# Kernel optimization log

Measured on AMD Instinct MI355X. Metric: run time of the kernel, lower is better.

Reference implementation:

```python
import jax, jax.numpy as jnp
import numpy as np

N_NODES = 10000
IN_SIZE, H_SIZE, OUT_SIZE = 512, 512, 64
N_EDGES = 163840


def gcn_conv(x, edge_index, W, b, n_nodes):
    """PyG-style GCNConv: add self-loops, sym-normalize, x @ W, scatter-add, + bias."""
    src, dst = edge_index[0], edge_index[1]
    loop = jnp.arange(n_nodes, dtype=src.dtype)
    src = jnp.concatenate([src, loop])
    dst = jnp.concatenate([dst, loop])
    # degree over destinations (self-loops included)
    deg = jax.ops.segment_sum(jnp.ones_like(dst, dtype=x.dtype), dst, num_segments=n_nodes)
    dinv = jnp.where(deg > 0, jax.lax.rsqrt(deg), 0.0)
    norm = dinv[src] * dinv[dst]                      # [E+N]
    h = x @ W                                          # [N, out]
    msg = h[src] * norm[:, None]                       # gather + scale
    out = jax.ops.segment_sum(msg, dst, num_segments=n_nodes)  # scatter-add
    return out + b


def setup_inputs() -> dict:
    key = jax.random.key(0)
    k = jax.random.split(key, 6)
    x = jax.random.normal(k[0], (N_NODES, IN_SIZE), dtype=jnp.float32)
    edge_index = jax.random.randint(k[1], (2, N_EDGES), 0, N_NODES, dtype=jnp.int64 if jax.config.read('jax_enable_x64') else jnp.int32)
    # Glorot-ish init for weights, zero bias (PyG default)
    W1 = jax.random.normal(k[2], (IN_SIZE, H_SIZE), dtype=jnp.float32) * (1.0 / np.sqrt(IN_SIZE))
    b1 = jnp.zeros((H_SIZE,), dtype=jnp.float32)
    W2 = jax.random.normal(k[3], (H_SIZE, OUT_SIZE), dtype=jnp.float32) * (1.0 / np.sqrt(H_SIZE))
    b2 = jnp.zeros((OUT_SIZE,), dtype=jnp.float32)
    return {"x": x, "edge_index": edge_index, "W1": W1, "b1": b1, "W2": W2, "b2": b2}


def reference(x, edge_index, W1, b1, W2, b2):
    n = x.shape[0]
    h = gcn_conv(x, edge_index, W1, b1, n)
    h = jax.nn.relu(h)
    h = gcn_conv(h, edge_index, W2, b2, n)
    return (h, jax.nn.log_softmax(h, axis=1))
```

## Files before the change

kernel.cpp:

```cpp
#include <hip/hip_runtime.h>
#include <math.h>

#define NN 10000
#define INF 512
#define HF  512
#define OF  64
#define NE  163840
#define MAXDEG 64

typedef __attribute__((ext_vector_type(8))) short bf16x8_t;
typedef __attribute__((ext_vector_type(4))) float f32x4_t;

__device__ inline ushort f2bf(float f) {
    unsigned u = __float_as_uint(f);
    u = (u + 0x7FFF + ((u >> 16) & 1)) >> 16;
    return (ushort)u;
}
__device__ inline float bf2f(ushort u) {
    return __uint_as_float(((unsigned)u) << 16);
}

#define GLL(gp, lp) __builtin_amdgcn_global_load_lds(                         \
    (const __attribute__((address_space(1))) unsigned int*)(gp),              \
    (__attribute__((address_space(3))) unsigned int*)(lp), 16, 0, 0)

#define CCB_X  2500
#define CCB_W1 2756
#define CCB_W2 2788
#define CCB_Z  2828
__global__ __launch_bounds__(256) void k_cvt(const float* __restrict__ X,
                                             ushort* __restrict__ Xb,
                                             const float* __restrict__ W1,
                                             ushort* __restrict__ W1T,
                                             const float* __restrict__ W2,
                                             ushort* __restrict__ W2T,
                                             int* __restrict__ gdeg) {
    __shared__ float tl[32][33];
    int b = blockIdx.x, t = threadIdx.x;
    if (b < CCB_X) {
        int i = (b * 256 + t) * 2;
        const float4* Xv = (const float4*)X;
        float4 v0 = Xv[i], v1 = Xv[i + 1];
        ushort4 o0, o1;
        o0.x = f2bf(v0.x); o0.y = f2bf(v0.y); o0.z = f2bf(v0.z); o0.w = f2bf(v0.w);
        o1.x = f2bf(v1.x); o1.y = f2bf(v1.y); o1.z = f2bf(v1.z); o1.w = f2bf(v1.w);
        ((ushort4*)Xb)[i] = o0;
        ((ushort4*)Xb)[i + 1] = o1;
    } else if (b < CCB_W2) {
        const float* W; ushort* WT; int N, tile;
        if (b < CCB_W1) { W = W1; WT = W1T; N = 512; tile = b - CCB_X; }
        else            { W = W2; WT = W2T; N = 64;  tile = b - CCB_W1; }
        int k0 = (tile & 15) * 32;
        int n0 = (tile >> 4) * 32;
        int tx = t & 31, ty = t >> 5;
#pragma unroll
        for (int i = 0; i < 4; i++)
            tl[ty + i * 8][tx] = W[(size_t)(k0 + ty + i * 8) * N + n0 + tx];
        __syncthreads();
#pragma unroll
        for (int i = 0; i < 4; i++)
            WT[(size_t)(n0 + ty + i * 8) * 512 + k0 + tx] = f2bf(tl[tx][ty + i * 8]);
    } else {
        int i = (b - CCB_W2) * 256 + t;
        if (i < NN) gdeg[i] = 0;
    }
}

#define GEMM_B 316
__global__ __launch_bounds__(256) void k_gemm_ell(const ushort* __restrict__ Xb,
                                                  const ushort* __restrict__ WT,
                                                  ushort* __restrict__ Y,
                                                  const int* __restrict__ src,
                                                  const int* __restrict__ dst,
                                                  int* __restrict__ gdeg,
                                                  int* __restrict__ ell, int E) {
    __shared__ ushort As[128 * 128];
    __shared__ ushort Bs[128 * 128];
    int b = blockIdx.x;
    int tid = threadIdx.x;
    if (b >= GEMM_B) {
        int e = (b - GEMM_B) * 256 + tid;
        if (e < E) {
            int s = src[e], d = dst[e];
            int r = atomicAdd(&gdeg[d], 1);
            if (r < MAXDEG) ell[d * MAXDEG + r] = s;
        }
        return;
    }
    int lane = tid & 63;
    int wave = tid >> 6;
    int m = lane & 15;
    int q = lane >> 4;
    int wr = wave >> 1;
    int wc = wave & 1;
    int row0 = (b % 79) * 128;
    int col0 = (b / 79) * 128;

    int lrow = lane >> 4;
    int p = lane & 15;
    int koff[4];
#pragma unroll
    for (int jm = 0; jm < 4; jm++) koff[jm] = (p ^ ((jm * 4 + lrow) & 15)) * 8;

    f32x4_t acc[4][4];
#pragma unroll
    for (int r = 0; r < 4; r++)
#pragma unroll
        for (int c = 0; c < 4; c++) acc[r][c] = (f32x4_t){0.f, 0.f, 0.f, 0.f};

    for (int kb = 0; kb < 512; kb += 128) {
#pragma unroll
        for (int j = 0; j < 8; j++) {
            int rloc = wave * 32 + j * 4;
            GLL(Xb + (size_t)(row0 + rloc + lrow) * 512 + kb + koff[j & 3],
                As + rloc * 128);
            GLL(WT + (size_t)(col0 + rloc + lrow) * 512 + kb + koff[j & 3],
                Bs + rloc * 128);
        }
        __syncthreads();
#pragma unroll
        for (int kc = 0; kc < 4; kc++) {
            bf16x8_t a[4], bb[4];
            int slot = ((kc * 4 + q) ^ m) * 8;
#pragma unroll
            for (int r = 0; r < 4; r++)
                a[r] = *(const bf16x8_t*)(As + (wr * 64 + r * 16 + m) * 128 + slot);
#pragma unroll
            for (int c = 0; c < 4; c++)
                bb[c] = *(const bf16x8_t*)(Bs + (wc * 64 + c * 16 + m) * 128 + slot);
#pragma unroll
            for (int r = 0; r < 4; r++)
#pragma unroll
                for (int c = 0; c < 4; c++)
                    acc[r][c] = __builtin_amdgcn_mfma_f32_16x16x32_bf16(a[r], bb[c], acc[r][c], 0, 0, 0);
        }
        __syncthreads();
    }
#pragma unroll
    for (int r = 0; r < 4; r++) {
#pragma unroll
        for (int c = 0; c < 4; c++) {
#pragma unroll
            for (int reg = 0; reg < 4; reg++) {
                int row = row0 + wr * 64 + r * 16 + q * 4 + reg;
                int col = col0 + wc * 64 + c * 16 + m;
                if (row < NN) Y[(size_t)row * 512 + col] = f2bf(acc[r][c][reg]);
            }
        }
    }
}

__global__ __launch_bounds__(256) void k_gemm64_mfma(const ushort* __restrict__ Ab,
                                                     const ushort* __restrict__ W2T,
                                                     ushort* __restrict__ Y) {
    __shared__ ushort As[64 * 128];
    __shared__ ushort Bs[64 * 128];
    int tid = threadIdx.x;
    int lane = tid & 63;
    int wave = tid >> 6;
    int m = lane & 15;
    int q = lane >> 4;
    int row0 = blockIdx.x * 64;

    int lrow = lane >> 4;
    int p = lane & 15;
    int koff[4];
#pragma unroll
    for (int jm = 0; jm < 4; jm++) koff[jm] = (p ^ ((jm * 4 + lrow) & 15)) * 8;

    f32x4_t acc[4];
#pragma unroll
    for (int c = 0; c < 4; c++) acc[c] = (f32x4_t){0.f, 0.f, 0.f, 0.f};

    for (int kb = 0; kb < 512; kb += 128) {
#pragma unroll
        for (int j = 0; j < 4; j++) {
            int rloc = wave * 16 + j * 4;
            GLL(Ab + (size_t)(row0 + rloc + lrow) * 512 + kb + koff[j],
                As + rloc * 128);
            GLL(W2T + (size_t)(rloc + lrow) * 512 + kb + koff[j],
                Bs + rloc * 128);
        }
        __syncthreads();
#pragma unroll
        for (int kc = 0; kc < 4; kc++) {
            int slot = ((kc * 4 + q) ^ m) * 8;
            bf16x8_t a = *(const bf16x8_t*)(As + (wave * 16 + m) * 128 + slot);
#pragma unroll
            for (int c = 0; c < 4; c++) {
                bf16x8_t bfr = *(const bf16x8_t*)(Bs + (c * 16 + m) * 128 + slot);
                acc[c] = __builtin_amdgcn_mfma_f32_16x16x32_bf16(a, bfr, acc[c], 0, 0, 0);
            }
        }
        __syncthreads();
    }
#pragma unroll
    for (int c = 0; c < 4; c++) {
#pragma unroll
        for (int reg = 0; reg < 4; reg++) {
            int row = row0 + wave * 16 + q * 4 + reg;
            int col = c * 16 + m;
            if (row < NN) Y[(size_t)row * 64 + col] = f2bf(acc[c][reg]);
        }
    }
}

__global__ __launch_bounds__(256) void k_agg1(const ushort* __restrict__ h1b,
                                              const int* __restrict__ gdeg,
                                              const int* __restrict__ ell,
                                              const float* __restrict__ b,
                                              ushort* __restrict__ a1b,
                                              float* __restrict__ wts) {
    __shared__ int   sidx[64];
    __shared__ float swt[64];
    int v = blockIdx.x;
    int t = threadIdx.x;
    int deg = gdeg[v]; if (deg > MAXDEG) deg = MAXDEG;
    float dv = rsqrtf((float)(deg + 1));
    if (t < 64) {
        int s = 0; float wt = 0.f;
        if (t < deg) {
            s = ell[v * MAXDEG + t];
            wt = rsqrtf((float)(gdeg[s] + 1)) * dv;
        }
        sidx[t] = s; swt[t] = wt;
        wts[v * MAXDEG + t] = wt;
    }
    __syncthreads();

    int fb = t * 2;
    float ax[8], ay[8];
#pragma unroll
    for (int k = 0; k < 8; k++) { ax[k] = 0.f; ay[k] = 0.f; }
    {
        ushort2 u = *(const ushort2*)(h1b + (size_t)v * 512 + fb);
        float dv2 = dv * dv;
        ax[0] = bf2f(u.x) * dv2;
        ay[0] = bf2f(u.y) * dv2;
    }
    int nr = (deg + 7) & ~7;
    for (int i = 0; i < nr; i += 8) {
        int   sK[8]; float wK[8];
#pragma unroll
        for (int k = 0; k < 8; k++) { sK[k] = sidx[i + k]; wK[k] = swt[i + k]; }
#pragma unroll
        for (int k = 0; k < 8; k++) {
            ushort2 u = *(const ushort2*)(h1b + (size_t)sK[k] * 512 + fb);
            ax[k] += bf2f(u.x) * wK[k];
            ay[k] += bf2f(u.y) * wK[k];
        }
    }
    float tx = ((ax[0] + ax[1]) + (ax[2] + ax[3])) + ((ax[4] + ax[5]) + (ax[6] + ax[7]));
    float ty = ((ay[0] + ay[1]) + (ay[2] + ay[3])) + ((ay[4] + ay[5]) + (ay[6] + ay[7]));
    tx += b[fb];
    ty += b[fb + 1];
    ushort2 o;
    o.x = f2bf(tx > 0.f ? tx : 0.f);
    o.y = f2bf(ty > 0.f ? ty : 0.f);
    *(ushort2*)(a1b + (size_t)v * 512 + fb) = o;
}

__global__ __launch_bounds__(256) void k_agg2_lsm(const ushort* __restrict__ h2b,
                                                  const int* __restrict__ gdeg,
                                                  const int* __restrict__ ell,
                                                  const float* __restrict__ wts,
                                                  const float* __restrict__ b,
                                                  float* __restrict__ out) {
    __shared__ int   sidx[4][64];
    __shared__ float swt[4][64];
    int t = threadIdx.x & 63;
    int w = threadIdx.x >> 6;
    int v = blockIdx.x * 4 + w;
    int deg = gdeg[v]; if (deg > MAXDEG) deg = MAXDEG;
    float dv = rsqrtf((float)(deg + 1));
    int   e_ = ell[v * MAXDEG + t];
    float w_ = wts[v * MAXDEG + t];
    sidx[w][t] = (t < deg) ? e_ : 0;
    swt[w][t]  = (t < deg) ? w_ : 0.f;

    float acc[8];
#pragma unroll
    for (int k = 0; k < 8; k++) acc[k] = 0.f;
    acc[0] = bf2f(h2b[(size_t)v * 64 + t]) * (dv * dv);

    int nr = (deg + 7) & ~7;
    for (int i = 0; i < nr; i += 8) {
        int   sK[8]; float wK[8];
#pragma unroll
        for (int k = 0; k < 8; k++) { sK[k] = sidx[w][i + k]; wK[k] = swt[w][i + k]; }
#pragma unroll
        for (int k = 0; k < 8; k++)
            acc[k] += bf2f(h2b[(size_t)sK[k] * 64 + t]) * wK[k];
    }
    float h = ((acc[0] + acc[1]) + (acc[2] + acc[3])) +
              ((acc[4] + acc[5]) + (acc[6] + acc[7]));
    h += b[t];
    out[(size_t)v * 64 + t] = h;
    float m = h;
#pragma unroll
    for (int off = 32; off >= 1; off >>= 1) m = fmaxf(m, __shfl_xor(m, off, 64));
    float e = expf(h - m);
    float ssum = e;
#pragma unroll
    for (int off = 32; off >= 1; off >>= 1) ssum += __shfl_xor(ssum, off, 64);
    out[(size_t)NN * OF + (size_t)v * 64 + t] = h - m - logf(ssum);
}


extern "C" void kernel_launch(void* const* d_in, const int* in_sizes, int n_in,
                              void* d_out, int out_size, void* d_ws, size_t ws_size,
                              hipStream_t stream) {
    const float* x  = (const float*)d_in[0];
    const int*   ei = (const int*)d_in[1];
    const float* W1 = (const float*)d_in[2];
    const float* b1 = (const float*)d_in[3];
    const float* W2 = (const float*)d_in[4];
    const float* b2 = (const float*)d_in[5];
    float* out = (float*)d_out;

    int E = in_sizes[1] / 2;
    const int* src = ei;
    const int* dst = ei + E;

    char* w = (char*)d_ws;
    auto carve = [&](size_t bytes) {
        char* p = w;
        w += (bytes + 255) & ~size_t(255);
        return p;
    };
    ushort* Xb     = (ushort*)carve((size_t)NN * 512 * 2);
    ushort* h1b    = (ushort*)carve((size_t)NN * 512 * 2);
    ushort* a1b    = (ushort*)carve((size_t)NN * 512 * 2);
    ushort* h2b    = (ushort*)carve((size_t)NN * 64 * 2);
    ushort* W1Tb   = (ushort*)carve((size_t)512 * 512 * 2);
    ushort* W2Tb   = (ushort*)carve((size_t)64 * 512 * 2);
    int*   gdeg    = (int*)carve((size_t)NN * 4);
    int*   ell     = (int*)carve((size_t)NN * MAXDEG * 4);
    float* wts     = (float*)carve((size_t)NN * MAXDEG * 4);
    (void)ws_size;

    int fillB = (E + 255) / 256;
    k_cvt<<<CCB_Z, 256, 0, stream>>>(x, Xb, W1, W1Tb, W2, W2Tb, gdeg);
    k_gemm_ell<<<GEMM_B + fillB, 256, 0, stream>>>(Xb, W1Tb, h1b, src, dst,
                                                   gdeg, ell, E);
    k_agg1<<<NN, 256, 0, stream>>>(h1b, gdeg, ell, b1, a1b, wts);
    k_gemm64_mfma<<<(NN + 63) / 64, 256, 0, stream>>>(a1b, W2Tb, h2b);
    k_agg2_lsm<<<NN / 4, 256, 0, stream>>>(h2b, gdeg, ell, wts, b2, out);
}
```

Before: 131.9 us.

## Map one wavefront per node in layer-1 aggregation with 16-byte gathers

The first aggregation kernel now assigns a single 64-lane wavefront to each node, two nodes per 128-thread block, instead of a 256-thread block per node. Each lane gathers 8 bf16 features with one 16-byte load in place of a 4-byte pair, and the neighbor loop is unrolled by 4. Because the index and weight tables are written and read within one wavefront, the block barrier is removed. This aims to cut per-edge load instruction count and block-level synchronization overhead, at the cost of fewer lanes per node and fewer independent accumulators for latency hiding.

```diff
diff --git a/kernel.cpp b/kernel.cpp
--- a/kernel.cpp
+++ b/kernel.cpp
@@ -205,59 +205,57 @@
     }
 }
 
-__global__ __launch_bounds__(256) void k_agg1(const ushort* __restrict__ h1b,
+__global__ __launch_bounds__(128) void k_agg1(const ushort* __restrict__ h1b,
                                               const int* __restrict__ gdeg,
                                               const int* __restrict__ ell,
                                               const float* __restrict__ b,
                                               ushort* __restrict__ a1b,
                                               float* __restrict__ wts) {
-    __shared__ int   sidx[64];
-    __shared__ float swt[64];
-    int v = blockIdx.x;
-    int t = threadIdx.x;
+    __shared__ int   sidx[2][64];
+    __shared__ float swt[2][64];
+    int w = threadIdx.x >> 6;
+    int t = threadIdx.x & 63;
+    int v = blockIdx.x * 2 + w;
     int deg = gdeg[v]; if (deg > MAXDEG) deg = MAXDEG;
     float dv = rsqrtf((float)(deg + 1));
-    if (t < 64) {
-        int s = 0; float wt = 0.f;
-        if (t < deg) {
-            s = ell[v * MAXDEG + t];
-            wt = rsqrtf((float)(gdeg[s] + 1)) * dv;
-        }
-        sidx[t] = s; swt[t] = wt;
-        wts[v * MAXDEG + t] = wt;
-    }
-    __syncthreads();
-
-    int fb = t * 2;
-    float ax[8], ay[8];
-#pragma unroll
-    for (int k = 0; k < 8; k++) { ax[k] = 0.f; ay[k] = 0.f; }
+    int s = 0; float wt = 0.f;
+    if (t < deg) {
+        s = ell[v * MAXDEG + t];
+        wt = rsqrtf((float)(gdeg[s] + 1)) * dv;
+    }
+    sidx[w][t] = s; swt[w][t] = wt;
+    wts[v * MAXDEG + t] = wt;
+
+    int fb = t * 8;
+    float acc[8];
     {
-        ushort2 u = *(const ushort2*)(h1b + (size_t)v * 512 + fb);
+        bf16x8_t su = *(const bf16x8_t*)(h1b + (size_t)v * 512 + fb);
         float dv2 = dv * dv;
-        ax[0] = bf2f(u.x) * dv2;
-        ay[0] = bf2f(u.y) * dv2;
-    }
-    int nr = (deg + 7) & ~7;
-    for (int i = 0; i < nr; i += 8) {
-        int   sK[8]; float wK[8];
-#pragma unroll
-        for (int k = 0; k < 8; k++) { sK[k] = sidx[i + k]; wK[k] = swt[i + k]; }
-#pragma unroll
-        for (int k = 0; k < 8; k++) {
-            ushort2 u = *(const ushort2*)(h1b + (size_t)sK[k] * 512 + fb);
-            ax[k] += bf2f(u.x) * wK[k];
-            ay[k] += bf2f(u.y) * wK[k];
-        }
-    }
-    float tx = ((ax[0] + ax[1]) + (ax[2] + ax[3])) + ((ax[4] + ax[5]) + (ax[6] + ax[7]));
-    float ty = ((ay[0] + ay[1]) + (ay[2] + ay[3])) + ((ay[4] + ay[5]) + (ay[6] + ay[7]));
-    tx += b[fb];
-    ty += b[fb + 1];
-    ushort2 o;
-    o.x = f2bf(tx > 0.f ? tx : 0.f);
-    o.y = f2bf(ty > 0.f ? ty : 0.f);
-    *(ushort2*)(a1b + (size_t)v * 512 + fb) = o;
+#pragma unroll
+        for (int f = 0; f < 8; f++) acc[f] = bf2f((ushort)su[f]) * dv2;
+    }
+    int nr = (deg + 3) & ~3;
+    for (int i = 0; i < nr; i += 4) {
+        bf16x8_t nb[4]; float wK[4];
+#pragma unroll
+        for (int k = 0; k < 4; k++) {
+            int sK = sidx[w][i + k];
+            wK[k] = swt[w][i + k];
+            nb[k] = *(const bf16x8_t*)(h1b + (size_t)sK * 512 + fb);
+        }
+#pragma unroll
+        for (int k = 0; k < 4; k++)
+#pragma unroll
+            for (int f = 0; f < 8; f++)
+                acc[f] += bf2f((ushort)nb[k][f]) * wK[k];
+    }
+    bf16x8_t o;
+#pragma unroll
+    for (int f = 0; f < 8; f++) {
+        float x = acc[f] + b[fb + f];
+        o[f] = (short)f2bf(x > 0.f ? x : 0.f);
+    }
+    *(bf16x8_t*)(a1b + (size_t)v * 512 + fb) = o;
 }
 
 __global__ __launch_bounds__(256) void k_agg2_lsm(const ushort* __restrict__ h2b,
@@ -343,7 +341,7 @@
     k_cvt<<<CCB_Z, 256, 0, stream>>>(x, Xb, W1, W1Tb, W2, W2Tb, gdeg);
     k_gemm_ell<<<GEMM_B + fillB, 256, 0, stream>>>(Xb, W1Tb, h1b, src, dst,
                                                    gdeg, ell, E);
-    k_agg1<<<NN, 256, 0, stream>>>(h1b, gdeg, ell, b1, a1b, wts);
+    k_agg1<<<NN / 2, 128, 0, stream>>>(h1b, gdeg, ell, b1, a1b, wts);
     k_gemm64_mfma<<<(NN + 63) / 64, 256, 0, stream>>>(a1b, W2Tb, h2b);
     k_agg2_lsm<<<NN / 4, 256, 0, stream>>>(h2b, gdeg, ell, wts, b2, out);
 }
```

After: 129.6 us. Within noise of the previous version (-1.7%).
